# Performance work log

Measured on AMD Instinct MI355X. Metric: run time of the kernel, lower is better.

## Reference

```python
import jax, jax.numpy as jnp
import numpy as np

B, T, D, H, L, V = 4, 1024, 1024, 16, 6, 32000
HS = D // H
FF = 4 * D
EPS = 1e-5


def setup_inputs() -> dict:
    key = jax.random.key(0)
    ks = jax.random.split(key, 16)
    s = 0.02
    n = lambda k, shape: (jax.random.normal(k, shape, jnp.float32) * s)
    return {
        'idx': jax.random.randint(ks[0], (B, T), 0, V),
        'targets': jax.random.randint(ks[1], (B, T), 0, V),
        'tok_emb': n(ks[2], (V, D)),
        'pos_emb': n(ks[3], (T, D)),
        'Wq': n(ks[4], (L, D, H, HS)),
        'Wk': n(ks[5], (L, D, H, HS)),
        'Wv': n(ks[6], (L, D, H, HS)),
        'proj_w': n(ks[7], (L, D, D)),
        'proj_b': jnp.zeros((L, D), jnp.float32),
        'ln1_g': jnp.ones((L, D), jnp.float32),
        'ln1_b': jnp.zeros((L, D), jnp.float32),
        'ln2_g': jnp.ones((L, D), jnp.float32),
        'ln2_b': jnp.zeros((L, D), jnp.float32),
        'ff_w1': n(ks[8], (L, D, FF)),
        'ff_b1': jnp.zeros((L, FF), jnp.float32),
        'ff_w2': n(ks[9], (L, FF, D)),
        'ff_b2': jnp.zeros((L, D), jnp.float32),
        'lnf_g': jnp.ones((D,), jnp.float32),
        'lnf_b': jnp.zeros((D,), jnp.float32),
        'head_w': n(ks[10], (D, V)),
        'head_b': jnp.zeros((V,), jnp.float32),
    }


def _ln(x, g, b):
    m = jnp.mean(x, axis=-1, keepdims=True)
    v = jnp.mean((x - m) ** 2, axis=-1, keepdims=True)
    return (x - m) * jax.lax.rsqrt(v + EPS) * g + b


def _forward(idx, targets, tok_emb, pos_emb, Wq, Wk, Wv, proj_w, proj_b,
             ln1_g, ln1_b, ln2_g, ln2_b, ff_w1, ff_b1, ff_w2, ff_b2,
             lnf_g, lnf_b, head_w, head_b):
    b, t = idx.shape
    x = tok_emb[idx] + pos_emb[:t]                       # [B,T,D]
    mask = jnp.tril(jnp.ones((t, t), bool))              # causal
    scale = jnp.float32(D) ** -0.5                       # NOTE: scales by num_dims (c), as in source
    for l in range(L):
        h = _ln(x, ln1_g[l], ln1_b[l])
        q = jnp.einsum('btd,dhs->bhts', h, Wq[l])        # [B,H,T,HS]
        k = jnp.einsum('btd,dhs->bhts', h, Wk[l])
        v = jnp.einsum('btd,dhs->bhts', h, Wv[l])
        w = jnp.einsum('bhts,bhus->bhtu', q, k) * scale  # [B,H,T,T]
        w = jnp.where(mask, w, -jnp.inf)
        w = jax.nn.softmax(w, axis=-1)
        o = jnp.einsum('bhtu,bhus->bhts', w, v)          # [B,H,T,HS]
        o = o.transpose(0, 2, 1, 3).reshape(b, t, D)     # concat heads
        x = x + jnp.einsum('btd,de->bte', o, proj_w[l]) + proj_b[l]
        h2 = _ln(x, ln2_g[l], ln2_b[l])
        ff = jax.nn.relu(jnp.einsum('btd,df->btf', h2, ff_w1[l]) + ff_b1[l])
        x = x + jnp.einsum('btf,fd->btd', ff, ff_w2[l]) + ff_b2[l]
    x = _ln(x, lnf_g, lnf_b)
    logits = jnp.einsum('btd,dv->btv', x, head_w) + head_b
    logits = logits.reshape(b * t, V)
    tgt = targets.reshape(b * t)
    logp = jax.nn.log_softmax(logits, axis=-1)
    loss = -jnp.mean(jnp.take_along_axis(logp, tgt[:, None], axis=-1))
    return logits, loss


def reference(idx, targets, tok_emb, pos_emb, Wq, Wk, Wv, proj_w, proj_b,
              ln1_g, ln1_b, ln2_g, ln2_b, ff_w1, ff_b1, ff_w2, ff_b2,
              lnf_g, lnf_b, head_w, head_b):
    return _forward(idx, targets, tok_emb, pos_emb, Wq, Wk, Wv, proj_w, proj_b,
                    ln1_g, ln1_b, ln2_g, ln2_b, ff_w1, ff_b1, ff_w2, ff_b2,
                    lnf_g, lnf_b, head_w, head_b)
```

## Files before the change

kernel.cpp:

```cpp
#include <hip/hip_runtime.h>

typedef __attribute__((ext_vector_type(8))) short bf16x8;
typedef __attribute__((ext_vector_type(4))) float f32x4;

#define L_LAYERS 6
#define T_SEQ 1024
#define D_MODEL 1024
#define N_HEAD 16
#define HS 64
#define FF_DIM 4096
#define VOCAB 32000
#define BT_ROWS 4096
#define ATTN_SCALE 0.03125f

__device__ __forceinline__ ushort f2bf(float f) {
  unsigned u = __builtin_bit_cast(unsigned, f);
  unsigned r = (u + 0x7fffu + ((u >> 16) & 1u)) >> 16;
  return (ushort)r;
}
__device__ __forceinline__ float waveRedSum(float v) {
#pragma unroll
  for (int off = 32; off; off >>= 1) v += __shfl_xor(v, off);
  return v;
}
__device__ __forceinline__ float waveRedMax(float v) {
#pragma unroll
  for (int off = 32; off; off >>= 1) v = fmaxf(v, __shfl_xor(v, off));
  return v;
}
__device__ __forceinline__ void gload16(const void* g, void* l) {
  __builtin_amdgcn_global_load_lds(
      (const __attribute__((address_space(1))) unsigned int*)g,
      (__attribute__((address_space(3))) unsigned int*)l, 16, 0, 0);
}

__global__ __launch_bounds__(256) void embed_kernel(const int* __restrict__ idx,
                                                    const float* __restrict__ tok,
                                                    const float* __restrict__ pos,
                                                    float* __restrict__ x) {
  int row = blockIdx.x;
  int tid = threadIdx.x;
  int t = row & (T_SEQ - 1);
  int id = idx[row];
  float4 tv = ((const float4*)(tok + (size_t)id * D_MODEL))[tid];
  float4 pv = ((const float4*)(pos + (size_t)t * D_MODEL))[tid];
  tv.x += pv.x; tv.y += pv.y; tv.z += pv.z; tv.w += pv.w;
  ((float4*)(x + (size_t)row * D_MODEL))[tid] = tv;
}

__global__ __launch_bounds__(256) void ln_kernel(const float* __restrict__ x,
                                                 const float* __restrict__ g,
                                                 const float* __restrict__ b,
                                                 ushort* __restrict__ out) {
  int row = blockIdx.x;
  int tid = threadIdx.x;
  __shared__ float red[4];
  float4 xv = ((const float4*)(x + (size_t)row * D_MODEL))[tid];
  float s = xv.x + xv.y + xv.z + xv.w;
  s = waveRedSum(s);
  if ((tid & 63) == 0) red[tid >> 6] = s;
  __syncthreads();
  float mean = (red[0] + red[1] + red[2] + red[3]) * (1.0f / D_MODEL);
  __syncthreads();
  float d0 = xv.x - mean, d1 = xv.y - mean, d2 = xv.z - mean, d3 = xv.w - mean;
  float v = d0 * d0 + d1 * d1 + d2 * d2 + d3 * d3;
  v = waveRedSum(v);
  if ((tid & 63) == 0) red[tid >> 6] = v;
  __syncthreads();
  float var = (red[0] + red[1] + red[2] + red[3]) * (1.0f / D_MODEL);
  float rstd = rsqrtf(var + 1e-5f);
  float4 gv = ((const float4*)g)[tid];
  float4 bv = ((const float4*)b)[tid];
  ushort4 o;
  o.x = f2bf(d0 * rstd * gv.x + bv.x);
  o.y = f2bf(d1 * rstd * gv.y + bv.y);
  o.z = f2bf(d2 * rstd * gv.z + bv.z);
  o.w = f2bf(d3 * rstd * gv.w + bv.w);
  ((ushort4*)(out + (size_t)row * D_MODEL))[tid] = o;
}

__device__ __forceinline__ void wconv_body(const float* __restrict__ W,
                                           ushort* __restrict__ WT,
                                           int Kd, int Nd, int n0, int k0) {
  __shared__ ushort tile[64][72];
  int tid = threadIdx.x;
#pragma unroll
  for (int i = 0; i < 4; i++) {
    int c = tid + i * 256;
    int row = c >> 4, cc = c & 15;
    float4 wv = *(const float4*)&W[(size_t)(k0 + row) * Nd + n0 + cc * 4];
    tile[row][cc * 4 + 0] = f2bf(wv.x);
    tile[row][cc * 4 + 1] = f2bf(wv.y);
    tile[row][cc * 4 + 2] = f2bf(wv.z);
    tile[row][cc * 4 + 3] = f2bf(wv.w);
  }
  __syncthreads();
#pragma unroll
  for (int i = 0; i < 2; i++) {
    int c = tid + i * 256;
    int n = c >> 3, kc = c & 7;
    __align__(16) ushort tmp[8];
#pragma unroll
    for (int j = 0; j < 8; j++) tmp[j] = tile[kc * 8 + j][n];
    *(int4*)&WT[(size_t)(n0 + n) * Kd + k0 + kc * 8] = *(const int4*)tmp;
  }
}

__global__ __launch_bounds__(256) void wconv_kernel(const float* __restrict__ W,
                                                    ushort* __restrict__ WT,
                                                    int Kd, int Nd) {
  wconv_body(W, WT, Kd, Nd, blockIdx.x * 64, blockIdx.y * 64);
}

__global__ __launch_bounds__(256) void wconv4_kernel(const float* __restrict__ W0,
                                                     const float* __restrict__ W1,
                                                     const float* __restrict__ W2,
                                                     const float* __restrict__ W3,
                                                     ushort* __restrict__ WT,
                                                     int Kd, int Nd) {
  int z = blockIdx.z;
  const float* W = (z == 0) ? W0 : (z == 1) ? W1 : (z == 2) ? W2 : W3;
  wconv_body(W, WT + (size_t)z * Kd * Nd, Kd, Nd, blockIdx.x * 64, blockIdx.y * 64);
}

__global__ __launch_bounds__(256) void vtrans_kernel(const ushort* __restrict__ v,
                                                     ushort* __restrict__ vT) {
  __shared__ ushort tile[64][72];
  int bh = blockIdx.y;
  int t0 = blockIdx.x * 64;
  int tid = threadIdx.x;
#pragma unroll
  for (int i = 0; i < 2; i++) {
    int c = tid + i * 256;
    int row = c >> 3, cc = c & 7;
    *(int4*)&tile[row][cc * 8] =
        *(const int4*)&v[((size_t)bh * T_SEQ + t0 + row) * HS + cc * 8];
  }
  __syncthreads();
#pragma unroll
  for (int i = 0; i < 2; i++) {
    int c = tid + i * 256;
    int hs = c >> 3, tc = c & 7;
    __align__(16) ushort tmp[8];
#pragma unroll
    for (int j = 0; j < 8; j++) tmp[j] = tile[tc * 8 + j][hs];
    *(int4*)&vT[((size_t)bh * HS + hs) * T_SEQ + t0 + tc * 8] = *(const int4*)tmp;
  }
}

template <int BM, int BN, int WM, int WN, int EPI>
__global__ __launch_bounds__(WM * WN * 64, 2) void gemmp_kernel(
    const ushort* __restrict__ A, const ushort* __restrict__ BT, int K,
    const float* __restrict__ bias, float* __restrict__ outf,
    ushort* __restrict__ outb, ushort* __restrict__ outk,
    ushort* __restrict__ outv, int ldo) {
  constexpr int PM = BM / WM, PN = BN / WN;
  constexpr int MR = PM / 16, NR = PN / 16;
  constexpr int ROWS = BM + BN;
  constexpr int NWAVES = WM * WN;
  constexpr int LPW = (ROWS / 8) / NWAVES;
  __shared__ __align__(16) ushort buf[2][ROWS * 64];
  int tid = threadIdx.x;
  int lane = tid & 63, wave = tid >> 6;
  int wm = wave / WN, wn = wave % WN;
  int a = lane & 15, gg = lane >> 4;
  int srow8 = lane >> 3;
  int scol8 = ((lane & 7) ^ (lane >> 3)) * 8;
  int m0 = blockIdx.y * BM, n0 = blockIdx.x * BN;
  f32x4 acc[MR][NR] = {};
  int nt = K >> 6;

  auto STAGE = [&](int t, int d) {
    int k0 = t * 64;
#pragma unroll
    for (int j = 0; j < LPW; j++) {
      int r0 = (wave * LPW + j) * 8;
      if (r0 < BM) {
        gload16(&A[(size_t)(m0 + r0 + srow8) * K + k0 + scol8], &buf[d][r0 * 64]);
      } else {
        gload16(&BT[(size_t)(n0 + (r0 - BM) + srow8) * K + k0 + scol8], &buf[d][r0 * 64]);
      }
    }
  };

  auto COMPUTE = [&](int d) {
    const ushort* bA = &buf[d][0];
    const ushort* bB = &buf[d][BM * 64];
#pragma unroll
    for (int s = 0; s < 2; s++) {
      bf16x8 af[MR], bfr[NR];
#pragma unroll
      for (int i = 0; i < MR; i++) {
        int row = wm * PM + i * 16 + a;
        af[i] = *(const bf16x8*)&bA[row * 64 + (((s * 4 + gg) ^ (a & 7)) * 8)];
      }
#pragma unroll
      for (int j = 0; j < NR; j++) {
        int row = wn * PN + j * 16 + a;
        bfr[j] = *(const bf16x8*)&bB[row * 64 + (((s * 4 + gg) ^ (a & 7)) * 8)];
      }
#pragma unroll
      for (int i = 0; i < MR; i++)
#pragma unroll
        for (int j = 0; j < NR; j++)
          acc[i][j] = __builtin_amdgcn_mfma_f32_16x16x32_bf16(af[i], bfr[j], acc[i][j], 0, 0, 0);
    }
  };

  STAGE(0, 0);
  __syncthreads();
  int cur = 0;
  for (int t = 0; t < nt; t++) {
    if (t + 1 < nt) STAGE(t + 1, cur ^ 1);
    COMPUTE(cur);
    __syncthreads();
    cur ^= 1;
  }

#pragma unroll
  for (int i = 0; i < MR; i++) {
#pragma unroll
    for (int j = 0; j < NR; j++) {
#pragma unroll
      for (int r = 0; r < 4; r++) {
        int mrow = m0 + wm * PM + i * 16 + gg * 4 + r;
        int ncol = n0 + wn * PN + j * 16 + a;
        float v = acc[i][j][r];
        if (EPI == 0) {
          int which = ncol >> 10;
          int n1 = ncol & 1023;
          int h = n1 >> 6, sidx = n1 & 63;
          int bb = mrow >> 10, tt = mrow & 1023;
          ushort* dst = (which == 0) ? outb : (which == 1) ? outk : outv;
          dst[(((size_t)(bb * N_HEAD + h)) * T_SEQ + tt) * HS + sidx] = f2bf(v);
        } else if (EPI == 1) {
          outf[(size_t)mrow * ldo + ncol] += v + bias[ncol];
        } else if (EPI == 2) {
          float t2 = v + bias[ncol];
          outb[(size_t)mrow * ldo + ncol] = f2bf(t2 > 0.0f ? t2 : 0.0f);
        } else {
          outf[(size_t)mrow * ldo + ncol] = v + bias[ncol];
        }
      }
    }
  }
}

__global__ __launch_bounds__(256) void attn_kernel(const ushort* __restrict__ q,
                                                   const ushort* __restrict__ k,
                                                   const ushort* __restrict__ vT,
                                                   ushort* __restrict__ o) {
  __shared__ __align__(16) ushort Ksm[64 * 72];
  __shared__ __align__(16) ushort Vsm[64 * 72];
  __shared__ __align__(16) ushort Psm[4][16 * 72];
  int tid = threadIdx.x;
  int lane = tid & 63, w = tid >> 6;
  int a = lane & 15, gg = lane >> 4;
  int qt = blockIdx.x, bh = blockIdx.y;
  int qrow_b = qt * 64 + w * 16;
  int qmy = qrow_b + a;

  bf16x8 qf[2];
  const ushort* qbase = q + ((size_t)bh * T_SEQ + qmy) * HS;
  qf[0] = *(const bf16x8*)&qbase[gg * 8];
  qf[1] = *(const bf16x8*)&qbase[32 + gg * 8];

  float m_run = -__builtin_inff();
  float l_run = 0.0f;
  f32x4 oacc[4] = {};
  int nkt = qt + 1;

  for (int kt = 0; kt < nkt; kt++) {
    int k0 = kt * 64;
    __syncthreads();
#pragma unroll
    for (int i = 0; i < 2; i++) {
      int c = tid + i * 256;
      int row = c >> 3, cc = c & 7;
      *(int4*)&Ksm[row * 72 + cc * 8] =
          *(const int4*)&k[((size_t)bh * T_SEQ + k0 + row) * HS + cc * 8];
      *(int4*)&Vsm[row * 72 + cc * 8] =
          *(const int4*)&vT[((size_t)bh * HS + row) * T_SEQ + k0 + cc * 8];
    }
    __syncthreads();

    f32x4 st[4] = {};
#pragma unroll
    for (int ku = 0; ku < 4; ku++) {
#pragma unroll
      for (int s = 0; s < 2; s++) {
        bf16x8 kf = *(const bf16x8*)&Ksm[(ku * 16 + a) * 72 + s * 32 + gg * 8];
        st[ku] = __builtin_amdgcn_mfma_f32_16x16x32_bf16(kf, qf[s], st[ku], 0, 0, 0);
      }
    }

    float pv[16];
    float pm = -__builtin_inff();
#pragma unroll
    for (int ku = 0; ku < 4; ku++) {
#pragma unroll
      for (int r = 0; r < 4; r++) {
        int u = k0 + ku * 16 + gg * 4 + r;
        float val = (u <= qmy) ? st[ku][r] * ATTN_SCALE : -__builtin_inff();
        pv[ku * 4 + r] = val;
        pm = fmaxf(pm, val);
      }
    }
    pm = fmaxf(pm, __shfl_xor(pm, 16));
    pm = fmaxf(pm, __shfl_xor(pm, 32));
    float m_new = fmaxf(m_run, pm);
    float cfac = expf(m_run - m_new);
    float tsum = 0.0f;
#pragma unroll
    for (int xi = 0; xi < 16; xi++) {
      float p = expf(pv[xi] - m_new);
      pv[xi] = p;
      tsum += p;
    }
    tsum += __shfl_xor(tsum, 16);
    tsum += __shfl_xor(tsum, 32);
    l_run = l_run * cfac + tsum;
    m_run = m_new;

    ushort* P = (ushort*)&Psm[w][0];
    asm volatile("s_waitcnt lgkmcnt(0)" ::: "memory");
#pragma unroll
    for (int ku = 0; ku < 4; ku++) {
      ushort4 pw;
      pw.x = f2bf(pv[ku * 4 + 0]);
      pw.y = f2bf(pv[ku * 4 + 1]);
      pw.z = f2bf(pv[ku * 4 + 2]);
      pw.w = f2bf(pv[ku * 4 + 3]);
      *(ushort4*)&P[a * 72 + ku * 16 + gg * 4] = pw;
    }
#pragma unroll
    for (int r = 0; r < 4; r++) {
      float cr = __shfl(cfac, gg * 4 + r);
#pragma unroll
      for (int nb = 0; nb < 4; nb++) oacc[nb][r] *= cr;
    }
    asm volatile("s_waitcnt lgkmcnt(0)" ::: "memory");
#pragma unroll
    for (int kb = 0; kb < 2; kb++) {
      bf16x8 pa = *(const bf16x8*)&P[a * 72 + kb * 32 + gg * 8];
#pragma unroll
      for (int nb = 0; nb < 4; nb++) {
        bf16x8 vb = *(const bf16x8*)&Vsm[(nb * 16 + a) * 72 + kb * 32 + gg * 8];
        oacc[nb] = __builtin_amdgcn_mfma_f32_16x16x32_bf16(pa, vb, oacc[nb], 0, 0, 0);
      }
    }
  }

  float linv = 1.0f / l_run;
  int bb = bh >> 4, hh = bh & 15;
#pragma unroll
  for (int r = 0; r < 4; r++) {
    float li = __shfl(linv, gg * 4 + r);
    int qr = qrow_b + gg * 4 + r;
#pragma unroll
    for (int nb = 0; nb < 4; nb++) {
      o[((size_t)(bb * T_SEQ + qr)) * D_MODEL + hh * HS + nb * 16 + a] =
          f2bf(oacc[nb][r] * li);
    }
  }
}

__global__ __launch_bounds__(256) void loss_row_kernel(const float* __restrict__ logits,
                                                       const int* __restrict__ tgt,
                                                       float* __restrict__ row_loss) {
  int row = blockIdx.x, tid = threadIdx.x;
  __shared__ float red[4];
  const float4* l4 = (const float4*)(logits + (size_t)row * VOCAB);
  float mx = -__builtin_inff();
  for (int i = tid; i < VOCAB / 4; i += 256) {
    float4 v = l4[i];
    mx = fmaxf(fmaxf(mx, fmaxf(v.x, v.y)), fmaxf(v.z, v.w));
  }
  mx = waveRedMax(mx);
  if ((tid & 63) == 0) red[tid >> 6] = mx;
  __syncthreads();
  mx = fmaxf(fmaxf(red[0], red[1]), fmaxf(red[2], red[3]));
  __syncthreads();
  float s = 0.0f;
  for (int i = tid; i < VOCAB / 4; i += 256) {
    float4 v = l4[i];
    s += expf(v.x - mx) + expf(v.y - mx) + expf(v.z - mx) + expf(v.w - mx);
  }
  s = waveRedSum(s);
  if ((tid & 63) == 0) red[tid >> 6] = s;
  __syncthreads();
  if (tid == 0) {
    float tot = red[0] + red[1] + red[2] + red[3];
    row_loss[row] = mx + logf(tot) - logits[(size_t)row * VOCAB + tgt[row]];
  }
}

__global__ __launch_bounds__(256) void loss_final_kernel(const float* __restrict__ row_loss,
                                                         float* __restrict__ out) {
  int tid = threadIdx.x;
  __shared__ float red[4];
  float s = 0.0f;
  for (int i = tid; i < BT_ROWS; i += 256) s += row_loss[i];
  s = waveRedSum(s);
  if ((tid & 63) == 0) red[tid >> 6] = s;
  __syncthreads();
  if (tid == 0) out[0] = (red[0] + red[1] + red[2] + red[3]) * (1.0f / BT_ROWS);
}

extern "C" void kernel_launch(void* const* d_in, const int* in_sizes, int n_in,
                              void* d_out, int out_size, void* d_ws, size_t ws_size,
                              hipStream_t stream) {
  const int* idx = (const int*)d_in[0];
  const int* tgt = (const int*)d_in[1];
  const float* tok_emb = (const float*)d_in[2];
  const float* pos_emb = (const float*)d_in[3];
  const float* Wq = (const float*)d_in[4];
  const float* Wk = (const float*)d_in[5];
  const float* Wv = (const float*)d_in[6];
  const float* proj_w = (const float*)d_in[7];
  const float* proj_b = (const float*)d_in[8];
  const float* ln1_g = (const float*)d_in[9];
  const float* ln1_b = (const float*)d_in[10];
  const float* ln2_g = (const float*)d_in[11];
  const float* ln2_b = (const float*)d_in[12];
  const float* ff_w1 = (const float*)d_in[13];
  const float* ff_b1 = (const float*)d_in[14];
  const float* ff_w2 = (const float*)d_in[15];
  const float* ff_b2 = (const float*)d_in[16];
  const float* lnf_g = (const float*)d_in[17];
  const float* lnf_b = (const float*)d_in[18];
  const float* head_w = (const float*)d_in[19];
  const float* head_b = (const float*)d_in[20];

  char* ws = (char*)d_ws;
  size_t off = 0;
  float* x = (float*)(ws + off); off += (size_t)BT_ROWS * D_MODEL * 4;
  ushort* h = (ushort*)(ws + off); off += (size_t)BT_ROWS * D_MODEL * 2;
  ushort* qb = (ushort*)(ws + off); off += (size_t)BT_ROWS * D_MODEL * 2;
  ushort* kb = (ushort*)(ws + off); off += (size_t)BT_ROWS * D_MODEL * 2;
  ushort* vb = (ushort*)(ws + off); off += (size_t)BT_ROWS * D_MODEL * 2;
  ushort* vTb = (ushort*)(ws + off); off += (size_t)BT_ROWS * D_MODEL * 2;
  ushort* ob = (ushort*)(ws + off); off += (size_t)BT_ROWS * D_MODEL * 2;
  ushort* ffb = (ushort*)(ws + off); off += (size_t)BT_ROWS * FF_DIM * 2;
  ushort* wqkvT = (ushort*)(ws + off); off += (size_t)4 * D_MODEL * D_MODEL * 2;
  ushort* wprojT = wqkvT + (size_t)3 * D_MODEL * D_MODEL;
  ushort* wff1T = (ushort*)(ws + off); off += (size_t)FF_DIM * D_MODEL * 2;
  ushort* wff2T = (ushort*)(ws + off); off += (size_t)D_MODEL * FF_DIM * 2;
  float* row_loss = (float*)(ws + off); off += (size_t)BT_ROWS * 4;
  ushort* headT = wqkvT;

  float* logits = (float*)d_out;

  embed_kernel<<<BT_ROWS, 256, 0, stream>>>(idx, tok_emb, pos_emb, x);

  for (int l = 0; l < L_LAYERS; l++) {
    size_t wo = (size_t)l * D_MODEL * D_MODEL;
    size_t fo = (size_t)l * D_MODEL * FF_DIM;
    wconv4_kernel<<<dim3(16, 16, 4), 256, 0, stream>>>(Wq + wo, Wk + wo, Wv + wo, proj_w + wo,
                                                       wqkvT, D_MODEL, D_MODEL);
    wconv_kernel<<<dim3(64, 16), 256, 0, stream>>>(ff_w1 + fo, wff1T, D_MODEL, FF_DIM);
    wconv_kernel<<<dim3(16, 64), 256, 0, stream>>>(ff_w2 + fo, wff2T, FF_DIM, D_MODEL);

    ln_kernel<<<BT_ROWS, 256, 0, stream>>>(x, ln1_g + l * D_MODEL, ln1_b + l * D_MODEL, h);
    gemmp_kernel<128, 128, 2, 2, 0><<<dim3(24, 32), 256, 0, stream>>>(
        h, wqkvT, D_MODEL, nullptr, nullptr, qb, kb, vb, 0);
    vtrans_kernel<<<dim3(16, 64), 256, 0, stream>>>(vb, vTb);
    attn_kernel<<<dim3(16, 64), 256, 0, stream>>>(qb, kb, vTb, ob);
    gemmp_kernel<128, 128, 2, 2, 1><<<dim3(8, 32), 256, 0, stream>>>(
        ob, wprojT, D_MODEL, proj_b + l * D_MODEL, x, nullptr, nullptr, nullptr, D_MODEL);
    ln_kernel<<<BT_ROWS, 256, 0, stream>>>(x, ln2_g + l * D_MODEL, ln2_b + l * D_MODEL, h);
    gemmp_kernel<256, 256, 2, 4, 2><<<dim3(16, 16), 512, 0, stream>>>(
        h, wff1T, D_MODEL, ff_b1 + (size_t)l * FF_DIM, nullptr, ffb, nullptr, nullptr, FF_DIM);
    gemmp_kernel<128, 128, 2, 2, 1><<<dim3(8, 32), 256, 0, stream>>>(
        ffb, wff2T, FF_DIM, ff_b2 + l * D_MODEL, x, nullptr, nullptr, nullptr, D_MODEL);
  }

  ln_kernel<<<BT_ROWS, 256, 0, stream>>>(x, lnf_g, lnf_b, h);

  for (int c = 0; c < 5; c++) {
    wconv_kernel<<<dim3(100, 16), 256, 0, stream>>>(head_w + c * 6400, headT, D_MODEL, VOCAB);
    gemmp_kernel<256, 256, 2, 4, 3><<<dim3(25, 16), 512, 0, stream>>>(
        h, headT, D_MODEL, head_b + c * 6400, logits + c * 6400, nullptr, nullptr, nullptr, VOCAB);
  }

  loss_row_kernel<<<BT_ROWS, 256, 0, stream>>>(logits, tgt, row_loss);
  loss_final_kernel<<<1, 256, 0, stream>>>(row_loss, logits + (size_t)BT_ROWS * VOCAB);
}
```

Before: 2.248 ms.

## Add 8-wave ping-pong GEMM for FF1 and LM head, single-pass online loss

Adds a 256x256 GEMM kernel with 8 waves, a double-buffered 128KB LDS, and half-tile staged loads interleaved with MFMA phases that use setprio and barriers. It replaces the FF1 GEMM and the five chunked head GEMMs. The head weight is now converted once into the larger qb region, so the head GEMM runs as one launch over all 32000 columns. The loss-row kernel becomes a single-pass online max/sum-exp, halving its reads of the logits. The new kernel relies on a large dynamic LDS allocation and hand-tuned vmcnt waits, which are fragile if the tile or launch sizes change.

```diff
diff --git a/kernel.cpp b/kernel.cpp
--- a/kernel.cpp
+++ b/kernel.cpp
@@ -21,11 +21,6 @@
 __device__ __forceinline__ float waveRedSum(float v) {
 #pragma unroll
   for (int off = 32; off; off >>= 1) v += __shfl_xor(v, off);
-  return v;
-}
-__device__ __forceinline__ float waveRedMax(float v) {
-#pragma unroll
-  for (int off = 32; off; off >>= 1) v = fmaxf(v, __shfl_xor(v, off));
   return v;
 }
 __device__ __forceinline__ void gload16(const void* g, void* l) {
@@ -246,6 +241,123 @@
   }
 }
 
+template <int EPI>
+__global__ __launch_bounds__(512, 2) void gemm8_kernel(
+    const ushort* __restrict__ A, const ushort* __restrict__ BT, int K,
+    const float* __restrict__ bias, float* __restrict__ outf,
+    ushort* __restrict__ outb, int ldo) {
+  extern __shared__ __align__(16) ushort lds[];
+  int tid = threadIdx.x;
+  int lane = tid & 63, wave = tid >> 6;
+  int wm = wave >> 1, wn = wave & 1;
+  int a = lane & 15, gg = lane >> 4;
+  int m0 = blockIdx.y * 256, n0 = blockIdx.x * 256;
+  int srow = lane >> 3;
+  int scol = ((lane & 7) ^ (lane >> 3)) * 8;
+  int nt = K >> 6;
+  f32x4 acc[4][8] = {};
+
+  auto stageH = [&](int t, int which) {
+    int d = t & 1;
+    int k0 = t * 64;
+    const ushort* src = (which < 2) ? A : BT;
+    int base0 = (which < 2) ? m0 : n0;
+    int rh = (which & 1) * 128;
+    ushort* dst = lds + ((which < 2) ? 0 : 32768) + d * 16384 + rh * 64;
+#pragma unroll
+    for (int q = 0; q < 2; q++) {
+      int r0 = wave * 16 + q * 8;
+      gload16(&src[(size_t)(base0 + rh + r0 + srow) * K + k0 + scol], dst + r0 * 64);
+    }
+  };
+
+  stageH(0, 0); stageH(0, 1); stageH(0, 2); stageH(0, 3);
+  if (nt > 1) { stageH(1, 0); stageH(1, 1); }
+  if (nt > 1) asm volatile("s_waitcnt vmcnt(4)" ::: "memory");
+  else        asm volatile("s_waitcnt vmcnt(0)" ::: "memory");
+  __builtin_amdgcn_s_barrier();
+
+  for (int t = 0; t < nt; t++) {
+    int d = t & 1;
+    const ushort* bA = lds + d * 16384;
+    const ushort* bB = lds + 32768 + d * 16384;
+    bf16x8 af[4][2], bf0[4][2];
+#pragma unroll
+    for (int i = 0; i < 4; i++)
+#pragma unroll
+      for (int s = 0; s < 2; s++) {
+        int row = wm * 64 + i * 16 + a;
+        af[i][s] = *(const bf16x8*)&bA[row * 64 + (((s * 4 + gg) ^ (a & 7)) * 8)];
+      }
+#pragma unroll
+    for (int j = 0; j < 4; j++)
+#pragma unroll
+      for (int s = 0; s < 2; s++) {
+        int row = wn * 128 + j * 16 + a;
+        bf0[j][s] = *(const bf16x8*)&bB[row * 64 + (((s * 4 + gg) ^ (a & 7)) * 8)];
+      }
+    if (t + 1 < nt) { stageH(t + 1, 2); stageH(t + 1, 3); }
+    __builtin_amdgcn_s_barrier();
+    __builtin_amdgcn_sched_barrier(0);
+    __builtin_amdgcn_s_setprio(1);
+#pragma unroll
+    for (int i = 0; i < 4; i++)
+#pragma unroll
+      for (int j = 0; j < 4; j++)
+#pragma unroll
+        for (int s = 0; s < 2; s++)
+          acc[i][j] = __builtin_amdgcn_mfma_f32_16x16x32_bf16(af[i][s], bf0[j][s], acc[i][j], 0, 0, 0);
+    __builtin_amdgcn_s_setprio(0);
+    __builtin_amdgcn_sched_barrier(0);
+    __builtin_amdgcn_s_barrier();
+    bf16x8 bf1[4][2];
+#pragma unroll
+    for (int j = 0; j < 4; j++)
+#pragma unroll
+      for (int s = 0; s < 2; s++) {
+        int row = wn * 128 + 64 + j * 16 + a;
+        bf1[j][s] = *(const bf16x8*)&bB[row * 64 + (((s * 4 + gg) ^ (a & 7)) * 8)];
+      }
+    if (t + 2 < nt) { stageH(t + 2, 0); stageH(t + 2, 1); }
+    __builtin_amdgcn_s_barrier();
+    __builtin_amdgcn_sched_barrier(0);
+    __builtin_amdgcn_s_setprio(1);
+#pragma unroll
+    for (int i = 0; i < 4; i++)
+#pragma unroll
+      for (int j = 0; j < 4; j++)
+#pragma unroll
+        for (int s = 0; s < 2; s++)
+          acc[i][j + 4] = __builtin_amdgcn_mfma_f32_16x16x32_bf16(af[i][s], bf1[j][s], acc[i][j + 4], 0, 0, 0);
+    __builtin_amdgcn_s_setprio(0);
+    __builtin_amdgcn_sched_barrier(0);
+    if (t + 1 < nt) {
+      if (t + 2 < nt) asm volatile("s_waitcnt vmcnt(4)" ::: "memory");
+      else            asm volatile("s_waitcnt vmcnt(0)" ::: "memory");
+    }
+    __builtin_amdgcn_s_barrier();
+  }
+
+#pragma unroll
+  for (int i = 0; i < 4; i++) {
+#pragma unroll
+    for (int j = 0; j < 8; j++) {
+#pragma unroll
+      for (int r = 0; r < 4; r++) {
+        int mrow = m0 + wm * 64 + i * 16 + gg * 4 + r;
+        int ncol = n0 + wn * 128 + j * 16 + a;
+        float v = acc[i][j][r];
+        if (EPI == 2) {
+          float t2 = v + bias[ncol];
+          outb[(size_t)mrow * ldo + ncol] = f2bf(t2 > 0.0f ? t2 : 0.0f);
+        } else {
+          outf[(size_t)mrow * ldo + ncol] = v + bias[ncol];
+        }
+      }
+    }
+  }
+}
+
 __global__ __launch_bounds__(256) void attn_kernel(const ushort* __restrict__ q,
                                                    const ushort* __restrict__ k,
                                                    const ushort* __restrict__ vT,
@@ -369,29 +481,29 @@
                                                        const int* __restrict__ tgt,
                                                        float* __restrict__ row_loss) {
   int row = blockIdx.x, tid = threadIdx.x;
-  __shared__ float red[4];
+  __shared__ float redm[4], reds[4];
   const float4* l4 = (const float4*)(logits + (size_t)row * VOCAB);
-  float mx = -__builtin_inff();
+  float m = -__builtin_inff(), s = 0.0f;
   for (int i = tid; i < VOCAB / 4; i += 256) {
     float4 v = l4[i];
-    mx = fmaxf(fmaxf(mx, fmaxf(v.x, v.y)), fmaxf(v.z, v.w));
-  }
-  mx = waveRedMax(mx);
-  if ((tid & 63) == 0) red[tid >> 6] = mx;
-  __syncthreads();
-  mx = fmaxf(fmaxf(red[0], red[1]), fmaxf(red[2], red[3]));
-  __syncthreads();
-  float s = 0.0f;
-  for (int i = tid; i < VOCAB / 4; i += 256) {
-    float4 v = l4[i];
-    s += expf(v.x - mx) + expf(v.y - mx) + expf(v.z - mx) + expf(v.w - mx);
-  }
-  s = waveRedSum(s);
-  if ((tid & 63) == 0) red[tid >> 6] = s;
+    float cm = fmaxf(fmaxf(v.x, v.y), fmaxf(v.z, v.w));
+    if (cm > m) { s *= expf(m - cm); m = cm; }
+    s += expf(v.x - m) + expf(v.y - m) + expf(v.z - m) + expf(v.w - m);
+  }
+#pragma unroll
+  for (int off = 32; off; off >>= 1) {
+    float om = __shfl_xor(m, off), os = __shfl_xor(s, off);
+    float nm = fmaxf(m, om);
+    s = s * expf(m - nm) + os * expf(om - nm);
+    m = nm;
+  }
+  if ((tid & 63) == 0) { redm[tid >> 6] = m; reds[tid >> 6] = s; }
   __syncthreads();
   if (tid == 0) {
-    float tot = red[0] + red[1] + red[2] + red[3];
-    row_loss[row] = mx + logf(tot) - logits[(size_t)row * VOCAB + tgt[row]];
+    float M = fmaxf(fmaxf(redm[0], redm[1]), fmaxf(redm[2], redm[3]));
+    float S = reds[0] * expf(redm[0] - M) + reds[1] * expf(redm[1] - M) +
+              reds[2] * expf(redm[2] - M) + reds[3] * expf(redm[3] - M);
+    row_loss[row] = M + logf(S) - logits[(size_t)row * VOCAB + tgt[row]];
   }
 }
 
@@ -447,7 +559,7 @@
   ushort* wff1T = (ushort*)(ws + off); off += (size_t)FF_DIM * D_MODEL * 2;
   ushort* wff2T = (ushort*)(ws + off); off += (size_t)D_MODEL * FF_DIM * 2;
   float* row_loss = (float*)(ws + off); off += (size_t)BT_ROWS * 4;
-  ushort* headT = wqkvT;
+  ushort* headT = qb;
 
   float* logits = (float*)d_out;
 
@@ -469,19 +581,17 @@
     gemmp_kernel<128, 128, 2, 2, 1><<<dim3(8, 32), 256, 0, stream>>>(
         ob, wprojT, D_MODEL, proj_b + l * D_MODEL, x, nullptr, nullptr, nullptr, D_MODEL);
     ln_kernel<<<BT_ROWS, 256, 0, stream>>>(x, ln2_g + l * D_MODEL, ln2_b + l * D_MODEL, h);
-    gemmp_kernel<256, 256, 2, 4, 2><<<dim3(16, 16), 512, 0, stream>>>(
-        h, wff1T, D_MODEL, ff_b1 + (size_t)l * FF_DIM, nullptr, ffb, nullptr, nullptr, FF_DIM);
+    gemm8_kernel<2><<<dim3(16, 16), 512, 131072, stream>>>(
+        h, wff1T, D_MODEL, ff_b1 + (size_t)l * FF_DIM, nullptr, ffb, FF_DIM);
     gemmp_kernel<128, 128, 2, 2, 1><<<dim3(8, 32), 256, 0, stream>>>(
         ffb, wff2T, FF_DIM, ff_b2 + l * D_MODEL, x, nullptr, nullptr, nullptr, D_MODEL);
   }
 
   ln_kernel<<<BT_ROWS, 256, 0, stream>>>(x, lnf_g, lnf_b, h);
 
-  for (int c = 0; c < 5; c++) {
-    wconv_kernel<<<dim3(100, 16), 256, 0, stream>>>(head_w + c * 6400, headT, D_MODEL, VOCAB);
-    gemmp_kernel<256, 256, 2, 4, 3><<<dim3(25, 16), 512, 0, stream>>>(
-        h, headT, D_MODEL, head_b + c * 6400, logits + c * 6400, nullptr, nullptr, nullptr, VOCAB);
-  }
+  wconv_kernel<<<dim3(500, 16), 256, 0, stream>>>(head_w, headT, D_MODEL, VOCAB);
+  gemm8_kernel<3><<<dim3(125, 16), 512, 131072, stream>>>(
+      h, headT, D_MODEL, head_b, logits, nullptr, VOCAB);
 
   loss_row_kernel<<<BT_ROWS, 256, 0, stream>>>(logits, tgt, row_loss);
   loss_final_kernel<<<1, 256, 0, stream>>>(row_loss, logits + (size_t)BT_ROWS * VOCAB);
```

Result: faster. 2.116 ms (-5.9%).
